# Optimization experiments

Hardware: AMD Instinct MI355X
Metric: run time of the kernel (lower is better)

Reference implementation:

```python
import jax, jax.numpy as jnp
import numpy as np

N_NODES = 100000
N_EDGES = 1600000
IN_CH = 128
DIM = 128
OUT_CH = 10
NUM_GRAPHS = 128
BN_EPS = 1e-5


def _bn_train(h, gamma, beta):
    # BatchNorm1d in training mode: batch statistics over the node axis
    mean = jnp.mean(h, axis=0)
    var = jnp.var(h, axis=0)
    return (h - mean) * jax.lax.rsqrt(var + BN_EPS) * gamma + beta


def _gin_conv(x, src, dst, W1, b1, gamma, beta, W2, b2):
    # GINConv with eps=0: nn(x + sum_{j in N(i)} x_j)
    agg = jax.ops.segment_sum(x[src], dst, num_segments=x.shape[0])  # [N, d]
    h = (x + agg) @ W1 + b1
    h = jax.nn.relu(_bn_train(h, gamma, beta))
    h = jax.nn.relu(h @ W2 + b2)
    return h


def setup_inputs() -> dict:
    key = jax.random.key(0)
    ks = jax.random.split(key, 16)
    s = 0.02
    inp = {
        "x": jax.random.normal(ks[0], (N_NODES, IN_CH), dtype=jnp.float32),
        "edge_index": jax.random.randint(ks[1], (2, N_EDGES), 0, N_NODES, dtype=jnp.int64),
        "batch": jnp.sort(jax.random.randint(ks[2], (N_NODES,), 0, NUM_GRAPHS, dtype=jnp.int64)),
        # conv1 MLP
        "W1a": jax.random.normal(ks[3], (IN_CH, DIM), dtype=jnp.float32) * s,
        "b1a": jnp.zeros((DIM,), jnp.float32),
        "ga": jnp.ones((DIM,), jnp.float32),
        "ba": jnp.zeros((DIM,), jnp.float32),
        "W2a": jax.random.normal(ks[4], (DIM, DIM), dtype=jnp.float32) * s,
        "b2a": jnp.zeros((DIM,), jnp.float32),
        # conv2 MLP
        "W1b": jax.random.normal(ks[5], (DIM, DIM), dtype=jnp.float32) * s,
        "b1b": jnp.zeros((DIM,), jnp.float32),
        "gb": jnp.ones((DIM,), jnp.float32),
        "bb": jnp.zeros((DIM,), jnp.float32),
        "W2b": jax.random.normal(ks[6], (DIM, DIM), dtype=jnp.float32) * s,
        "b2b": jnp.zeros((DIM,), jnp.float32),
        # readout linears
        "Wl1": jax.random.normal(ks[7], (DIM, DIM), dtype=jnp.float32) * s,
        "bl1": jnp.zeros((DIM,), jnp.float32),
        "Wl2": jax.random.normal(ks[8], (DIM, OUT_CH), dtype=jnp.float32) * s,
        "bl2": jnp.zeros((OUT_CH,), jnp.float32),
    }
    return inp


def reference(x, edge_index, batch, W1a, b1a, ga, ba, W2a, b2a,
              W1b, b1b, gb, bb, W2b, b2b, Wl1, bl1, Wl2, bl2):
    src, dst = edge_index[0], edge_index[1]
    h = _gin_conv(x, src, dst, W1a, b1a, ga, ba, W2a, b2a)
    h = _gin_conv(h, src, dst, W1b, b1b, gb, bb, W2b, b2b)
    pooled = jax.ops.segment_sum(h, batch, num_segments=NUM_GRAPHS)  # [G, d]
    out = jax.nn.relu(pooled @ Wl1 + bl1)
    # dropout p=0.5 is identity in deterministic/eval evaluation
    out = out @ Wl2 + bl2
    return out
```

## Files before the change

### kernel.cpp

```cpp
#include <hip/hip_runtime.h>

#define N_NODES    100000
#define N_EDGES    1600000
#define DIM        128
#define OUT_CH     10
#define NUM_GRAPHS 128
#define BN_EPS     1e-5f

#define BSHIFT   10
#define NB       98
#define CAP      24576
#define SLICES   3
#define SLICE_SLOTS 8192

typedef __attribute__((ext_vector_type(8))) short short8;
typedef __attribute__((ext_vector_type(4))) float floatx4;

__device__ inline float bf2f(unsigned short u) {
    union { unsigned i; float f; } v; v.i = (unsigned)u << 16; return v.f;
}
__device__ inline unsigned short f2bf(float f) {
    union { float f; unsigned i; } v; v.f = f;
    unsigned r = (v.i + 0x7fffu + ((v.i >> 16) & 1u)) >> 16;
    return (unsigned short)r;
}

__global__ __launch_bounds__(256)
void k_bucket(const int* __restrict__ src, const int* __restrict__ dst,
              int* __restrict__ gcur, uint2* __restrict__ pairs) {
    __shared__ int h[NB];
    int t = threadIdx.x;
    if (t < NB) h[t] = 0;
    __syncthreads();
    int base = blockIdx.x * 4096;
    #pragma unroll
    for (int i = 0; i < 16; ++i) {
        int idx = base + i * 256 + t;
        if (idx < N_EDGES) atomicAdd(&h[dst[idx] >> BSHIFT], 1);
    }
    __syncthreads();
    if (t < NB) h[t] = atomicAdd(&gcur[t], h[t]);
    __syncthreads();
    #pragma unroll
    for (int i = 0; i < 16; ++i) {
        int idx = base + i * 256 + t;
        if (idx < N_EDGES) {
            int d = dst[idx];
            int b = d >> BSHIFT;
            int pos = atomicAdd(&h[b], 1);
            if (pos < CAP) pairs[(size_t)b * CAP + pos] = make_uint2((unsigned)src[idx], (unsigned)d);
        }
    }
}

__global__ __launch_bounds__(256)
void k_count2(const uint2* __restrict__ pairs, const int* __restrict__ gcur,
              int* __restrict__ cnt) {
    __shared__ int lc[1024];
    int bi = blockIdx.x / SLICES, s = blockIdx.x % SLICES;
    int t = threadIdx.x;
    for (int i = t; i < 1024; i += 256) lc[i] = 0;
    __syncthreads();
    int n  = min(gcur[bi], CAP);
    int lo = s * SLICE_SLOTS, hi = min(lo + SLICE_SLOTS, n);
    const uint2* P = pairs + (size_t)bi * CAP;
    for (int i = lo + t; i < hi; i += 256)
        atomicAdd(&lc[P[i].y & 1023], 1);
    __syncthreads();
    int nb0 = bi << BSHIFT;
    for (int i = t; i < 1024; i += 256)
        if (lc[i] > 0) atomicAdd(&cnt[nb0 + i], lc[i]);
}

__global__ __launch_bounds__(256)
void k_fill2(const uint2* __restrict__ pairs, const int* __restrict__ gcur,
             int* __restrict__ cursor, int* __restrict__ col) {
    __shared__ int lc[1024];
    __shared__ int lb[1024];
    int bi = blockIdx.x / SLICES, s = blockIdx.x % SLICES;
    int t = threadIdx.x;
    for (int i = t; i < 1024; i += 256) lc[i] = 0;
    __syncthreads();
    int n  = min(gcur[bi], CAP);
    int lo = s * SLICE_SLOTS, hi = min(lo + SLICE_SLOTS, n);
    const uint2* P = pairs + (size_t)bi * CAP;
    int nb0 = bi << BSHIFT;
    for (int i = lo + t; i < hi; i += 256)
        atomicAdd(&lc[P[i].y & 1023], 1);
    __syncthreads();
    for (int i = t; i < 1024; i += 256)
        lb[i] = (lc[i] > 0) ? atomicAdd(&cursor[nb0 + i], lc[i]) : 0;
    __syncthreads();
    for (int i = lo + t; i < hi; i += 256) {
        uint2 e = P[i];
        int p = atomicAdd(&lb[e.y & 1023], 1);
        col[p] = (int)e.x;
    }
}

__global__ void k_scanA(const int* __restrict__ cnt, int* __restrict__ outv,
                        int* __restrict__ bsum) {
    __shared__ int sh[256];
    int t = threadIdx.x;
    int base = blockIdx.x * 1024 + t * 4;
    int v0=0,v1=0,v2=0,v3=0;
    if (base+0 < N_NODES) v0 = cnt[base+0];
    if (base+1 < N_NODES) v1 = cnt[base+1];
    if (base+2 < N_NODES) v2 = cnt[base+2];
    if (base+3 < N_NODES) v3 = cnt[base+3];
    int s = v0+v1+v2+v3;
    sh[t] = s; __syncthreads();
    for (int off = 1; off < 256; off <<= 1) {
        int tmp = (t >= off) ? sh[t-off] : 0;
        __syncthreads();
        sh[t] += tmp;
        __syncthreads();
    }
    int excl = sh[t] - s;
    if (t == 255) bsum[blockIdx.x] = sh[255];
    int run = excl;
    if (base+0 < N_NODES) { outv[base+0] = run; run += v0; }
    if (base+1 < N_NODES) { outv[base+1] = run; run += v1; }
    if (base+2 < N_NODES) { outv[base+2] = run; run += v2; }
    if (base+3 < N_NODES) { outv[base+3] = run; run += v3; }
}

__global__ void k_scanB(int* __restrict__ bsum, int* __restrict__ row_ptr) {
    if (threadIdx.x == 0 && blockIdx.x == 0) {
        int run = 0;
        for (int i = 0; i < 98; ++i) { int v = bsum[i]; bsum[i] = run; run += v; }
        row_ptr[N_NODES] = run;
    }
}

__global__ void k_scanC(int* __restrict__ row_ptr, const int* __restrict__ bsum,
                        int* __restrict__ cursor) {
    int i = blockIdx.x * 256 + threadIdx.x;
    if (i < N_NODES) {
        int v = row_ptr[i] + bsum[i >> 10];
        row_ptr[i] = v;
        cursor[i]  = v;
    }
}

__global__ void k_cvt_x(const float* __restrict__ x, unsigned short* __restrict__ xb) {
    int idx = blockIdx.x * 256 + threadIdx.x;
    float4 v = ((const float4*)x)[idx];
    ushort4 o;
    o.x = f2bf(v.x); o.y = f2bf(v.y); o.z = f2bf(v.z); o.w = f2bf(v.w);
    ((ushort4*)xb)[idx] = o;
}

__global__ void k_prep_w(const float* __restrict__ W0, const float* __restrict__ W1,
                         const float* __restrict__ W2, const float* __restrict__ W3,
                         unsigned short* __restrict__ Wt) {
    const float* Ws[4] = {W0, W1, W2, W3};
    const float* W = Ws[blockIdx.y];
    unsigned short* o = Wt + blockIdx.y * (DIM * DIM);
    int idx = blockIdx.x * 256 + threadIdx.x;
    int n = idx >> 7, k = idx & 127;
    o[idx] = f2bf(W[k * DIM + n]);
}

__global__ void k_agg(const unsigned short* __restrict__ X,
                      unsigned short* __restrict__ Out,
                      const int* __restrict__ row_ptr, const int* __restrict__ col) {
    int wid = (blockIdx.x * 256 + threadIdx.x) >> 6;
    if (wid >= N_NODES) return;
    int lane = threadIdx.x & 63;
    int half = lane >> 5, m = lane & 31;
    const ushort4* X4 = (const ushort4*)X;

    float a0=0.f,a1=0.f,a2=0.f,a3=0.f;
    float c0=0.f,c1=0.f,c2=0.f,c3=0.f;
    if (half == 0) {
        ushort4 sv = X4[(size_t)wid * 32 + m];
        a0 = bf2f(sv.x); a1 = bf2f(sv.y); a2 = bf2f(sv.z); a3 = bf2f(sv.w);
    }
    int s = row_ptr[wid], e = row_ptr[wid + 1];
    int p = s + half;
    for (; p + 6 < e; p += 8) {
        int n0 = col[p], n1 = col[p + 2], n2 = col[p + 4], n3 = col[p + 6];
        ushort4 v0 = X4[(size_t)n0 * 32 + m];
        ushort4 v1 = X4[(size_t)n1 * 32 + m];
        ushort4 v2 = X4[(size_t)n2 * 32 + m];
        ushort4 v3 = X4[(size_t)n3 * 32 + m];
        a0 += bf2f(v0.x); a1 += bf2f(v0.y); a2 += bf2f(v0.z); a3 += bf2f(v0.w);
        c0 += bf2f(v1.x); c1 += bf2f(v1.y); c2 += bf2f(v1.z); c3 += bf2f(v1.w);
        a0 += bf2f(v2.x); a1 += bf2f(v2.y); a2 += bf2f(v2.z); a3 += bf2f(v2.w);
        c0 += bf2f(v3.x); c1 += bf2f(v3.y); c2 += bf2f(v3.z); c3 += bf2f(v3.w);
    }
    for (; p < e; p += 2) {
        ushort4 v = X4[(size_t)col[p] * 32 + m];
        a0 += bf2f(v.x); a1 += bf2f(v.y); a2 += bf2f(v.z); a3 += bf2f(v.w);
    }
    a0 += c0; a1 += c1; a2 += c2; a3 += c3;
    a0 += __shfl_xor(a0, 32);
    a1 += __shfl_xor(a1, 32);
    a2 += __shfl_xor(a2, 32);
    a3 += __shfl_xor(a3, 32);
    if (half == 0) {
        ushort4 o;
        o.x = f2bf(a0); o.y = f2bf(a1); o.z = f2bf(a2); o.w = f2bf(a3);
        ((ushort4*)Out)[(size_t)wid * 32 + m] = o;
    }
}

template<bool BN_LOAD, bool RELU_ST>
__global__ __launch_bounds__(256)
void k_gemm(const unsigned short* __restrict__ In, unsigned short* __restrict__ Out,
            const unsigned short* __restrict__ Wt, const float* __restrict__ bias,
            const float* __restrict__ scale, const float* __restrict__ shift) {
    __shared__ __align__(16) unsigned short sA[128][136];
    __shared__ __align__(16) unsigned short sB[128][136];

    int t  = threadIdx.x;
    int r0 = blockIdx.x * 128;

    #pragma unroll
    for (int u = 0; u < 8; ++u) {
        int f   = u * 256 + t;
        int row = f >> 4, kq = f & 15;
        int gr  = r0 + row;
        short8 v = {};
        if (gr < N_NODES) v = *(const short8*)(In + (size_t)gr * 128 + kq * 8);
        if (BN_LOAD) {
            #pragma unroll
            for (int j = 0; j < 8; ++j) {
                int k = kq * 8 + j;
                float fv = bf2f((unsigned short)v[j]);
                fv = fmaxf(fv * scale[k] + shift[k], 0.f);
                v[j] = (short)f2bf(fv);
            }
        }
        *(short8*)&sA[row][kq * 8] = v;
    }
    #pragma unroll
    for (int u = 0; u < 8; ++u) {
        int f = u * 256 + t;
        int n = f >> 4, kq = f & 15;
        *(short8*)&sB[n][kq * 8] = *(const short8*)(Wt + n * 128 + kq * 8);
    }
    __syncthreads();

    int wave = t >> 6;
    int lane = t & 63;
    int m = lane & 15;
    int q = lane >> 4;

    floatx4 acc[2][8] = {};
    #pragma unroll
    for (int kc = 0; kc < 128; kc += 32) {
        short8 n0 = *(const short8*)&sA[wave * 32 + m     ][kc + q * 8];
        short8 n1 = *(const short8*)&sA[wave * 32 + 16 + m][kc + q * 8];
        #pragma unroll
        for (int c = 0; c < 8; ++c) {
            short8 wf = *(const short8*)&sB[c * 16 + m][kc + q * 8];
            acc[0][c] = __builtin_amdgcn_mfma_f32_16x16x32_bf16(wf, n0, acc[0][c], 0, 0, 0);
            acc[1][c] = __builtin_amdgcn_mfma_f32_16x16x32_bf16(wf, n1, acc[1][c], 0, 0, 0);
        }
    }

    #pragma unroll
    for (int c = 0; c < 8; ++c) {
        int ch0 = c * 16 + q * 4;
        float4 bv = *(const float4*)(bias + ch0);
        #pragma unroll
        for (int h = 0; h < 2; ++h) {
            int node = r0 + wave * 32 + h * 16 + m;
            if (node < N_NODES) {
                float v0 = acc[h][c][0] + bv.x;
                float v1 = acc[h][c][1] + bv.y;
                float v2 = acc[h][c][2] + bv.z;
                float v3 = acc[h][c][3] + bv.w;
                if (RELU_ST) {
                    v0 = fmaxf(v0, 0.f); v1 = fmaxf(v1, 0.f);
                    v2 = fmaxf(v2, 0.f); v3 = fmaxf(v3, 0.f);
                }
                ushort4 o;
                o.x = f2bf(v0); o.y = f2bf(v1); o.z = f2bf(v2); o.w = f2bf(v3);
                *(ushort4*)(Out + (size_t)node * 128 + ch0) = o;
            }
        }
    }
}

#define ST_BLOCKS 250
#define ST_ROWS   400
__global__ __launch_bounds__(256)
void k_stats(const unsigned short* __restrict__ H,
             float* __restrict__ ssum, float* __restrict__ ssq) {
    __shared__ float rs[8][128];
    __shared__ float rq[8][128];
    int t  = threadIdx.x;
    int cq = t & 31;
    int r  = t >> 5;
    int row0 = blockIdx.x * ST_ROWS;
    float s0=0,s1=0,s2=0,s3=0,q0=0,q1=0,q2=0,q3=0;
    for (int i = r; i < ST_ROWS; i += 8) {
        ushort4 v = *(const ushort4*)(H + (size_t)(row0 + i) * 128 + cq * 4);
        float f0=bf2f(v.x), f1=bf2f(v.y), f2=bf2f(v.z), f3=bf2f(v.w);
        s0+=f0; s1+=f1; s2+=f2; s3+=f3;
        q0+=f0*f0; q1+=f1*f1; q2+=f2*f2; q3+=f3*f3;
    }
    rs[r][cq*4+0]=s0; rs[r][cq*4+1]=s1; rs[r][cq*4+2]=s2; rs[r][cq*4+3]=s3;
    rq[r][cq*4+0]=q0; rq[r][cq*4+1]=q1; rq[r][cq*4+2]=q2; rq[r][cq*4+3]=q3;
    __syncthreads();
    if (t < 128) {
        float a = 0.f, b = 0.f;
        #pragma unroll
        for (int j = 0; j < 8; ++j) { a += rs[j][t]; b += rq[j][t]; }
        atomicAdd(&ssum[t], a);
        atomicAdd(&ssq [t], b);
    }
}

__global__ void k_bnfin(const float* __restrict__ sum, const float* __restrict__ sq,
                        const float* __restrict__ gamma, const float* __restrict__ beta,
                        float* __restrict__ scale, float* __restrict__ shift) {
    int c = threadIdx.x;
    if (c < DIM) {
        float m   = sum[c] * (1.0f / N_NODES);
        float var = sq[c] * (1.0f / N_NODES) - m * m;
        float inv = rsqrtf(var + BN_EPS);
        float sc  = gamma[c] * inv;
        scale[c] = sc;
        shift[c] = beta[c] - m * sc;
    }
}

#define POOL_BLOCKS 512
#define POOL_CHUNK  196
__global__ void k_pool(const unsigned short* __restrict__ h, const int* __restrict__ batch,
                       float* __restrict__ pooled) {
    int c  = threadIdx.x;
    int n0 = blockIdx.x * POOL_CHUNK;
    if (n0 >= N_NODES) return;
    int n1 = min(n0 + POOL_CHUNK, N_NODES);
    int g = batch[n0];
    float acc = 0.f;
    for (int i = n0; i < n1; ++i) {
        int gi = batch[i];
        if (gi != g) { atomicAdd(&pooled[g * DIM + c], acc); acc = 0.f; g = gi; }
        acc += bf2f(h[(size_t)i * DIM + c]);
    }
    atomicAdd(&pooled[g * DIM + c], acc);
}

__global__ void k_readout1(const float* __restrict__ pooled, const float* __restrict__ W,
                           const float* __restrict__ b, float* __restrict__ r1) {
    int idx = blockIdx.x * 256 + threadIdx.x;
    int g = idx >> 7, c = idx & 127;
    float s = b[c];
    const float* p = pooled + g * DIM;
    #pragma unroll 8
    for (int k = 0; k < DIM; ++k) s += p[k] * W[k * DIM + c];
    r1[idx] = fmaxf(s, 0.f);
}

__global__ void k_readout2(const float* __restrict__ r1, const float* __restrict__ W,
                           const float* __restrict__ b, float* __restrict__ out) {
    int idx = blockIdx.x * 256 + threadIdx.x;
    if (idx >= NUM_GRAPHS * OUT_CH) return;
    int g = idx / OUT_CH, c = idx % OUT_CH;
    float s = b[c];
    const float* r = r1 + g * DIM;
    #pragma unroll 8
    for (int k = 0; k < DIM; ++k) s += r[k] * W[k * OUT_CH + c];
    out[idx] = s;
}

extern "C" void kernel_launch(void* const* d_in, const int* in_sizes, int n_in,
                              void* d_out, int out_size, void* d_ws, size_t ws_size,
                              hipStream_t stream) {
    const float* x   = (const float*)d_in[0];
    const int*   ei  = (const int*)d_in[1];
    const int*   bat = (const int*)d_in[2];
    const float* W1a = (const float*)d_in[3];
    const float* b1a = (const float*)d_in[4];
    const float* ga  = (const float*)d_in[5];
    const float* ba  = (const float*)d_in[6];
    const float* W2a = (const float*)d_in[7];
    const float* b2a = (const float*)d_in[8];
    const float* W1b = (const float*)d_in[9];
    const float* b1b = (const float*)d_in[10];
    const float* gb  = (const float*)d_in[11];
    const float* bbt = (const float*)d_in[12];
    const float* W2b = (const float*)d_in[13];
    const float* b2b = (const float*)d_in[14];
    const float* Wl1 = (const float*)d_in[15];
    const float* bl1 = (const float*)d_in[16];
    const float* Wl2 = (const float*)d_in[17];
    const float* bl2 = (const float*)d_in[18];
    float* out = (float*)d_out;

    const int* src = ei;
    const int* dst = ei + N_EDGES;

    char* w = (char*)d_ws;
    size_t off = 0;
    auto alloc = [&](size_t bytes) -> char* {
        char* p = w + off; off += (bytes + 255) & ~(size_t)255; return p;
    };
    unsigned short* xb   = (unsigned short*)alloc((size_t)N_NODES * DIM * 2);
    unsigned short* nb0  = (unsigned short*)alloc((size_t)N_NODES * DIM * 2);
    unsigned short* nb1  = (unsigned short*)alloc((size_t)N_NODES * DIM * 2);
    unsigned short* Wtb  = (unsigned short*)alloc((size_t)4 * DIM * DIM * 2);
    uint2* pairs   = (uint2*)alloc((size_t)NB * CAP * 8);
    int*   row_ptr = (int*)  alloc((size_t)(N_NODES + 1) * 4);
    int*   cnt     = (int*)  alloc((size_t)(NB * 1024) * 4);
    int*   cursor  = (int*)  alloc((size_t)N_NODES * 4);
    int*   col     = (int*)  alloc((size_t)N_EDGES * 4);
    int*   gcur    = (int*)  alloc(NB * 4);
    int*   bsum    = (int*)  alloc(98 * 4);
    float* ssumA   = (float*)alloc(DIM * 4);
    float* ssqA    = (float*)alloc(DIM * 4);
    float* ssumB   = (float*)alloc(DIM * 4);
    float* ssqB    = (float*)alloc(DIM * 4);
    float* scale   = (float*)alloc(DIM * 4);
    float* shift   = (float*)alloc(DIM * 4);
    float* pooled  = (float*)alloc((size_t)NUM_GRAPHS * DIM * 4);
    float* r1      = (float*)alloc((size_t)NUM_GRAPHS * DIM * 4);

    hipMemsetAsync(gcur,  0, NB * 4, stream);
    hipMemsetAsync(cnt,   0, (size_t)(NB * 1024) * 4, stream);
    hipMemsetAsync(ssumA, 0, DIM * 4 * 4, stream);
    hipMemsetAsync(pooled,0, (size_t)NUM_GRAPHS * DIM * 4, stream);

    k_bucket<<<(N_EDGES + 4095) / 4096, 256, 0, stream>>>(src, dst, gcur, pairs);
    k_count2<<<NB * SLICES, 256, 0, stream>>>(pairs, gcur, cnt);
    k_scanA<<<98, 256, 0, stream>>>(cnt, row_ptr, bsum);
    k_scanB<<<1, 64, 0, stream>>>(bsum, row_ptr);
    k_scanC<<<(N_NODES + 255) / 256, 256, 0, stream>>>(row_ptr, bsum, cursor);
    k_fill2<<<NB * SLICES, 256, 0, stream>>>(pairs, gcur, cursor, col);

    k_cvt_x<<<(N_NODES * DIM / 4) / 256, 256, 0, stream>>>(x, xb);
    k_prep_w<<<dim3(64, 4), 256, 0, stream>>>(W1a, W2a, W1b, W2b, Wtb);
    const unsigned short* Wt1a = Wtb;
    const unsigned short* Wt2a = Wtb + DIM * DIM;
    const unsigned short* Wt1b = Wtb + 2 * DIM * DIM;
    const unsigned short* Wt2b = Wtb + 3 * DIM * DIM;

    int agg_blocks  = (N_NODES * 64) / 256;
    int gemm_blocks = (N_NODES + 127) / 128;

    k_agg<<<agg_blocks, 256, 0, stream>>>(xb, nb0, row_ptr, col);
    k_gemm<false, false><<<gemm_blocks, 256, 0, stream>>>(nb0, nb1, Wt1a, b1a,
                                                          nullptr, nullptr);
    k_stats<<<ST_BLOCKS, 256, 0, stream>>>(nb1, ssumA, ssqA);
    k_bnfin<<<1, 128, 0, stream>>>(ssumA, ssqA, ga, ba, scale, shift);
    k_gemm<true, true><<<gemm_blocks, 256, 0, stream>>>(nb1, nb0, Wt2a, b2a,
                                                        scale, shift);
    k_agg<<<agg_blocks, 256, 0, stream>>>(nb0, nb1, row_ptr, col);
    k_gemm<false, false><<<gemm_blocks, 256, 0, stream>>>(nb1, nb0, Wt1b, b1b,
                                                          nullptr, nullptr);
    k_stats<<<ST_BLOCKS, 256, 0, stream>>>(nb0, ssumB, ssqB);
    k_bnfin<<<1, 128, 0, stream>>>(ssumB, ssqB, gb, bbt, scale, shift);
    k_gemm<true, true><<<gemm_blocks, 256, 0, stream>>>(nb0, nb1, Wt2b, b2b,
                                                        scale, shift);
    k_pool<<<POOL_BLOCKS, 128, 0, stream>>>(nb1, bat, pooled);
    k_readout1<<<(NUM_GRAPHS * DIM) / 256, 256, 0, stream>>>(pooled, Wl1, bl1, r1);
    k_readout2<<<(NUM_GRAPHS * OUT_CH + 255) / 256, 256, 0, stream>>>(r1, Wl2, bl2, out);
}
```

Measured before the change: 536.3 us.

## Simplify CSR build with finer buckets and async swizzled LDS loads in GEMM

New measurement: 526.3 us. No clear change (-1.9%).

```diff
diff --git a/kernel.cpp b/kernel.cpp
--- a/kernel.cpp
+++ b/kernel.cpp
@@ -7,11 +7,9 @@
 #define NUM_GRAPHS 128
 #define BN_EPS     1e-5f
 
-#define BSHIFT   10
-#define NB       98
-#define CAP      24576
-#define SLICES   3
-#define SLICE_SLOTS 8192
+#define BSHIFT   8
+#define NB2      391
+#define CAP2     5120
 
 typedef __attribute__((ext_vector_type(8))) short short8;
 typedef __attribute__((ext_vector_type(4))) float floatx4;
@@ -25,12 +23,18 @@
     return (unsigned short)r;
 }
 
+__device__ inline void async_cp16(const unsigned short* g, unsigned short* l) {
+    __builtin_amdgcn_global_load_lds(
+        (const __attribute__((address_space(1))) void*)g,
+        (__attribute__((address_space(3))) void*)l, 16, 0, 0);
+}
+
 __global__ __launch_bounds__(256)
 void k_bucket(const int* __restrict__ src, const int* __restrict__ dst,
               int* __restrict__ gcur, uint2* __restrict__ pairs) {
-    __shared__ int h[NB];
+    __shared__ int h[NB2];
     int t = threadIdx.x;
-    if (t < NB) h[t] = 0;
+    for (int i = t; i < NB2; i += 256) h[i] = 0;
     __syncthreads();
     int base = blockIdx.x * 4096;
     #pragma unroll
@@ -39,7 +43,7 @@
         if (idx < N_EDGES) atomicAdd(&h[dst[idx] >> BSHIFT], 1);
     }
     __syncthreads();
-    if (t < NB) h[t] = atomicAdd(&gcur[t], h[t]);
+    for (int i = t; i < NB2; i += 256) h[i] = atomicAdd(&gcur[i], h[i]);
     __syncthreads();
     #pragma unroll
     for (int i = 0; i < 16; ++i) {
@@ -48,98 +52,59 @@
             int d = dst[idx];
             int b = d >> BSHIFT;
             int pos = atomicAdd(&h[b], 1);
-            if (pos < CAP) pairs[(size_t)b * CAP + pos] = make_uint2((unsigned)src[idx], (unsigned)d);
+            if (pos < CAP2) pairs[(size_t)b * CAP2 + pos] = make_uint2((unsigned)src[idx], (unsigned)d);
         }
     }
 }
 
-__global__ __launch_bounds__(256)
-void k_count2(const uint2* __restrict__ pairs, const int* __restrict__ gcur,
-              int* __restrict__ cnt) {
-    __shared__ int lc[1024];
-    int bi = blockIdx.x / SLICES, s = blockIdx.x % SLICES;
+__global__ void k_bscan(const int* __restrict__ gcur, int* __restrict__ bbase,
+                        int* __restrict__ row_ptr) {
+    __shared__ int sh[512];
     int t = threadIdx.x;
-    for (int i = t; i < 1024; i += 256) lc[i] = 0;
-    __syncthreads();
-    int n  = min(gcur[bi], CAP);
-    int lo = s * SLICE_SLOTS, hi = min(lo + SLICE_SLOTS, n);
-    const uint2* P = pairs + (size_t)bi * CAP;
-    for (int i = lo + t; i < hi; i += 256)
-        atomicAdd(&lc[P[i].y & 1023], 1);
-    __syncthreads();
-    int nb0 = bi << BSHIFT;
-    for (int i = t; i < 1024; i += 256)
-        if (lc[i] > 0) atomicAdd(&cnt[nb0 + i], lc[i]);
-}
-
-__global__ __launch_bounds__(256)
-void k_fill2(const uint2* __restrict__ pairs, const int* __restrict__ gcur,
-             int* __restrict__ cursor, int* __restrict__ col) {
-    __shared__ int lc[1024];
-    __shared__ int lb[1024];
-    int bi = blockIdx.x / SLICES, s = blockIdx.x % SLICES;
-    int t = threadIdx.x;
-    for (int i = t; i < 1024; i += 256) lc[i] = 0;
-    __syncthreads();
-    int n  = min(gcur[bi], CAP);
-    int lo = s * SLICE_SLOTS, hi = min(lo + SLICE_SLOTS, n);
-    const uint2* P = pairs + (size_t)bi * CAP;
-    int nb0 = bi << BSHIFT;
-    for (int i = lo + t; i < hi; i += 256)
-        atomicAdd(&lc[P[i].y & 1023], 1);
-    __syncthreads();
-    for (int i = t; i < 1024; i += 256)
-        lb[i] = (lc[i] > 0) ? atomicAdd(&cursor[nb0 + i], lc[i]) : 0;
-    __syncthreads();
-    for (int i = lo + t; i < hi; i += 256) {
-        uint2 e = P[i];
-        int p = atomicAdd(&lb[e.y & 1023], 1);
-        col[p] = (int)e.x;
-    }
-}
-
-__global__ void k_scanA(const int* __restrict__ cnt, int* __restrict__ outv,
-                        int* __restrict__ bsum) {
-    __shared__ int sh[256];
-    int t = threadIdx.x;
-    int base = blockIdx.x * 1024 + t * 4;
-    int v0=0,v1=0,v2=0,v3=0;
-    if (base+0 < N_NODES) v0 = cnt[base+0];
-    if (base+1 < N_NODES) v1 = cnt[base+1];
-    if (base+2 < N_NODES) v2 = cnt[base+2];
-    if (base+3 < N_NODES) v3 = cnt[base+3];
-    int s = v0+v1+v2+v3;
-    sh[t] = s; __syncthreads();
-    for (int off = 1; off < 256; off <<= 1) {
-        int tmp = (t >= off) ? sh[t-off] : 0;
+    int v = (t < NB2) ? min(gcur[t], CAP2) : 0;
+    sh[t] = v; __syncthreads();
+    for (int off = 1; off < 512; off <<= 1) {
+        int tmp = (t >= off) ? sh[t - off] : 0;
         __syncthreads();
         sh[t] += tmp;
         __syncthreads();
     }
-    int excl = sh[t] - s;
-    if (t == 255) bsum[blockIdx.x] = sh[255];
-    int run = excl;
-    if (base+0 < N_NODES) { outv[base+0] = run; run += v0; }
-    if (base+1 < N_NODES) { outv[base+1] = run; run += v1; }
-    if (base+2 < N_NODES) { outv[base+2] = run; run += v2; }
-    if (base+3 < N_NODES) { outv[base+3] = run; run += v3; }
-}
-
-__global__ void k_scanB(int* __restrict__ bsum, int* __restrict__ row_ptr) {
-    if (threadIdx.x == 0 && blockIdx.x == 0) {
-        int run = 0;
-        for (int i = 0; i < 98; ++i) { int v = bsum[i]; bsum[i] = run; run += v; }
-        row_ptr[N_NODES] = run;
-    }
-}
-
-__global__ void k_scanC(int* __restrict__ row_ptr, const int* __restrict__ bsum,
-                        int* __restrict__ cursor) {
-    int i = blockIdx.x * 256 + threadIdx.x;
-    if (i < N_NODES) {
-        int v = row_ptr[i] + bsum[i >> 10];
-        row_ptr[i] = v;
-        cursor[i]  = v;
+    if (t < NB2) bbase[t] = sh[t] - v;
+    if (t == NB2 - 1) { bbase[NB2] = sh[t]; row_ptr[N_NODES] = sh[t]; }
+}
+
+__global__ __launch_bounds__(256)
+void k_csr(const uint2* __restrict__ pairs, const int* __restrict__ gcur,
+           const int* __restrict__ bbase, int* __restrict__ row_ptr,
+           int* __restrict__ col) {
+    __shared__ int hist[256];
+    __shared__ int cur[256];
+    int bi = blockIdx.x, t = threadIdx.x;
+    hist[t] = 0; __syncthreads();
+    int n = min(gcur[bi], CAP2);
+    const uint2* P = pairs + (size_t)bi * CAP2;
+    for (int i = t; i < n; i += 256)
+        atomicAdd(&hist[P[i].y & 255], 1);
+    __syncthreads();
+    int self = hist[t];
+    cur[t] = self; __syncthreads();
+    for (int off = 1; off < 256; off <<= 1) {
+        int tmp = (t >= off) ? cur[t - off] : 0;
+        __syncthreads();
+        cur[t] += tmp;
+        __syncthreads();
+    }
+    int excl = cur[t] - self;
+    int base = bbase[bi];
+    int node = (bi << 8) + t;
+    if (node < N_NODES) row_ptr[node] = base + excl;
+    __syncthreads();
+    cur[t] = base + excl;
+    __syncthreads();
+    for (int i = t; i < n; i += 256) {
+        uint2 e = P[i];
+        int pos = atomicAdd(&cur[e.y & 255], 1);
+        col[pos] = (int)e.x;
     }
 }
 
@@ -206,58 +171,52 @@
     }
 }
 
-template<bool BN_LOAD, bool RELU_ST>
+template<bool RELU_ST>
 __global__ __launch_bounds__(256)
 void k_gemm(const unsigned short* __restrict__ In, unsigned short* __restrict__ Out,
-            const unsigned short* __restrict__ Wt, const float* __restrict__ bias,
-            const float* __restrict__ scale, const float* __restrict__ shift) {
-    __shared__ __align__(16) unsigned short sA[128][136];
-    __shared__ __align__(16) unsigned short sB[128][136];
-
-    int t  = threadIdx.x;
+            const unsigned short* __restrict__ Wt, const float* __restrict__ bias) {
+    __shared__ __align__(16) unsigned short sA[128 * 128];
+    __shared__ __align__(16) unsigned short sB[128 * 128];
+
+    int t = threadIdx.x;
+    int w = t >> 6, lane = t & 63;
     int r0 = blockIdx.x * 128;
 
     #pragma unroll
     for (int u = 0; u < 8; ++u) {
-        int f   = u * 256 + t;
-        int row = f >> 4, kq = f & 15;
-        int gr  = r0 + row;
-        short8 v = {};
-        if (gr < N_NODES) v = *(const short8*)(In + (size_t)gr * 128 + kq * 8);
-        if (BN_LOAD) {
-            #pragma unroll
-            for (int j = 0; j < 8; ++j) {
-                int k = kq * 8 + j;
-                float fv = bf2f((unsigned short)v[j]);
-                fv = fmaxf(fv * scale[k] + shift[k], 0.f);
-                v[j] = (short)f2bf(fv);
-            }
-        }
-        *(short8*)&sA[row][kq * 8] = v;
+        int i = (w * 8 + u) * 64 + lane;
+        int row = i >> 4, p = i & 15;
+        int gr = r0 + row; if (gr >= N_NODES) gr = 0;
+        const unsigned short* g = In + (size_t)gr * 128 + ((p ^ (row & 7)) << 3);
+        async_cp16(g, sA + (size_t)(w * 8 + u) * 512);
     }
     #pragma unroll
     for (int u = 0; u < 8; ++u) {
-        int f = u * 256 + t;
-        int n = f >> 4, kq = f & 15;
-        *(short8*)&sB[n][kq * 8] = *(const short8*)(Wt + n * 128 + kq * 8);
-    }
-    __syncthreads();
-
-    int wave = t >> 6;
-    int lane = t & 63;
+        int i = (w * 8 + u) * 64 + lane;
+        int n = i >> 4, p = i & 15;
+        const unsigned short* g = Wt + n * 128 + ((p ^ (n & 7)) << 3);
+        async_cp16(g, sB + (size_t)(w * 8 + u) * 512);
+    }
+    __syncthreads();
+
     int m = lane & 15;
     int q = lane >> 4;
+    int sw = m & 7;
 
     floatx4 acc[2][8] = {};
-    #pragma unroll
-    for (int kc = 0; kc < 128; kc += 32) {
-        short8 n0 = *(const short8*)&sA[wave * 32 + m     ][kc + q * 8];
-        short8 n1 = *(const short8*)&sA[wave * 32 + 16 + m][kc + q * 8];
+    int rA0 = w * 32 + m, rA1 = w * 32 + 16 + m;
+    #pragma unroll
+    for (int kk = 0; kk < 4; ++kk) {
+        int cl = kk * 4 + q;
+        int cp = cl ^ sw;
+        short8 a0 = *(const short8*)&sA[rA0 * 128 + (cp << 3)];
+        short8 a1 = *(const short8*)&sA[rA1 * 128 + (cp << 3)];
         #pragma unroll
         for (int c = 0; c < 8; ++c) {
-            short8 wf = *(const short8*)&sB[c * 16 + m][kc + q * 8];
-            acc[0][c] = __builtin_amdgcn_mfma_f32_16x16x32_bf16(wf, n0, acc[0][c], 0, 0, 0);
-            acc[1][c] = __builtin_amdgcn_mfma_f32_16x16x32_bf16(wf, n1, acc[1][c], 0, 0, 0);
+            int nr = c * 16 + m;
+            short8 b = *(const short8*)&sB[nr * 128 + (cp << 3)];
+            acc[0][c] = __builtin_amdgcn_mfma_f32_16x16x32_bf16(b, a0, acc[0][c], 0, 0, 0);
+            acc[1][c] = __builtin_amdgcn_mfma_f32_16x16x32_bf16(b, a1, acc[1][c], 0, 0, 0);
         }
     }
 
@@ -267,7 +226,7 @@
         float4 bv = *(const float4*)(bias + ch0);
         #pragma unroll
         for (int h = 0; h < 2; ++h) {
-            int node = r0 + wave * 32 + h * 16 + m;
+            int node = r0 + w * 32 + h * 16 + m;
             if (node < N_NODES) {
                 float v0 = acc[h][c][0] + bv.x;
                 float v1 = acc[h][c][1] + bv.y;
@@ -327,6 +286,25 @@
         scale[c] = sc;
         shift[c] = beta[c] - m * sc;
     }
+}
+
+__global__ __launch_bounds__(256)
+void k_bn_apply(unsigned short* __restrict__ H, const float* __restrict__ scale,
+                const float* __restrict__ shift) {
+    __shared__ float ssc[128], ssh[128];
+    int t = threadIdx.x;
+    if (t < 128) { ssc[t] = scale[t]; ssh[t] = shift[t]; }
+    __syncthreads();
+    size_t idx = (size_t)blockIdx.x * 256 + t;
+    int k0 = ((int)idx & 15) * 8;
+    short8 v = ((short8*)H)[idx];
+    #pragma unroll
+    for (int j = 0; j < 8; ++j) {
+        float f = bf2f((unsigned short)v[j]);
+        f = fmaxf(f * ssc[k0 + j] + ssh[k0 + j], 0.f);
+        v[j] = (short)f2bf(f);
+    }
+    ((short8*)H)[idx] = v;
 }
 
 #define POOL_BLOCKS 512
@@ -406,13 +384,11 @@
     unsigned short* nb0  = (unsigned short*)alloc((size_t)N_NODES * DIM * 2);
     unsigned short* nb1  = (unsigned short*)alloc((size_t)N_NODES * DIM * 2);
     unsigned short* Wtb  = (unsigned short*)alloc((size_t)4 * DIM * DIM * 2);
-    uint2* pairs   = (uint2*)alloc((size_t)NB * CAP * 8);
+    uint2* pairs   = (uint2*)alloc((size_t)NB2 * CAP2 * 8);
     int*   row_ptr = (int*)  alloc((size_t)(N_NODES + 1) * 4);
-    int*   cnt     = (int*)  alloc((size_t)(NB * 1024) * 4);
-    int*   cursor  = (int*)  alloc((size_t)N_NODES * 4);
     int*   col     = (int*)  alloc((size_t)N_EDGES * 4);
-    int*   gcur    = (int*)  alloc(NB * 4);
-    int*   bsum    = (int*)  alloc(98 * 4);
+    int*   gcur    = (int*)  alloc((NB2 + 1) * 4);
+    int*   bbase   = (int*)  alloc((NB2 + 1) * 4);
     float* ssumA   = (float*)alloc(DIM * 4);
     float* ssqA    = (float*)alloc(DIM * 4);
     float* ssumB   = (float*)alloc(DIM * 4);
@@ -422,17 +398,13 @@
     float* pooled  = (float*)alloc((size_t)NUM_GRAPHS * DIM * 4);
     float* r1      = (float*)alloc((size_t)NUM_GRAPHS * DIM * 4);
 
-    hipMemsetAsync(gcur,  0, NB * 4, stream);
-    hipMemsetAsync(cnt,   0, (size_t)(NB * 1024) * 4, stream);
+    hipMemsetAsync(gcur,  0, (NB2 + 1) * 4, stream);
     hipMemsetAsync(ssumA, 0, DIM * 4 * 4, stream);
     hipMemsetAsync(pooled,0, (size_t)NUM_GRAPHS * DIM * 4, stream);
 
     k_bucket<<<(N_EDGES + 4095) / 4096, 256, 0, stream>>>(src, dst, gcur, pairs);
-    k_count2<<<NB * SLICES, 256, 0, stream>>>(pairs, gcur, cnt);
-    k_scanA<<<98, 256, 0, stream>>>(cnt, row_ptr, bsum);
-    k_scanB<<<1, 64, 0, stream>>>(bsum, row_ptr);
-    k_scanC<<<(N_NODES + 255) / 256, 256, 0, stream>>>(row_ptr, bsum, cursor);
-    k_fill2<<<NB * SLICES, 256, 0, stream>>>(pairs, gcur, cursor, col);
+    k_bscan<<<1, 512, 0, stream>>>(gcur, bbase, row_ptr);
+    k_csr<<<NB2, 256, 0, stream>>>(pairs, gcur, bbase, row_ptr, col);
 
     k_cvt_x<<<(N_NODES * DIM / 4) / 256, 256, 0, stream>>>(x, xb);
     k_prep_w<<<dim3(64, 4), 256, 0, stream>>>(W1a, W2a, W1b, W2b, Wtb);
@@ -443,21 +415,20 @@
 
     int agg_blocks  = (N_NODES * 64) / 256;
     int gemm_blocks = (N_NODES + 127) / 128;
+    int bn_blocks   = (N_NODES * DIM / 8) / 256;
 
     k_agg<<<agg_blocks, 256, 0, stream>>>(xb, nb0, row_ptr, col);
-    k_gemm<false, false><<<gemm_blocks, 256, 0, stream>>>(nb0, nb1, Wt1a, b1a,
-                                                          nullptr, nullptr);
+    k_gemm<false><<<gemm_blocks, 256, 0, stream>>>(nb0, nb1, Wt1a, b1a);
     k_stats<<<ST_BLOCKS, 256, 0, stream>>>(nb1, ssumA, ssqA);
     k_bnfin<<<1, 128, 0, stream>>>(ssumA, ssqA, ga, ba, scale, shift);
-    k_gemm<true, true><<<gemm_blocks, 256, 0, stream>>>(nb1, nb0, Wt2a, b2a,
-                                                        scale, shift);
+    k_bn_apply<<<bn_blocks, 256, 0, stream>>>(nb1, scale, shift);
+    k_gemm<true><<<gemm_blocks, 256, 0, stream>>>(nb1, nb0, Wt2a, b2a);
     k_agg<<<agg_blocks, 256, 0, stream>>>(nb0, nb1, row_ptr, col);
-    k_gemm<false, false><<<gemm_blocks, 256, 0, stream>>>(nb1, nb0, Wt1b, b1b,
-                                                          nullptr, nullptr);
+    k_gemm<false><<<gemm_blocks, 256, 0, stream>>>(nb1, nb0, Wt1b, b1b);
     k_stats<<<ST_BLOCKS, 256, 0, stream>>>(nb0, ssumB, ssqB);
     k_bnfin<<<1, 128, 0, stream>>>(ssumB, ssqB, gb, bbt, scale, shift);
-    k_gemm<true, true><<<gemm_blocks, 256, 0, stream>>>(nb0, nb1, Wt2b, b2b,
-                                                        scale, shift);
+    k_bn_apply<<<bn_blocks, 256, 0, stream>>>(nb0, scale, shift);
+    k_gemm<true><<<gemm_blocks, 256, 0, stream>>>(nb0, nb1, Wt2b, b2b);
     k_pool<<<POOL_BLOCKS, 128, 0, stream>>>(nb1, bat, pooled);
     k_readout1<<<(NUM_GRAPHS * DIM) / 256, 256, 0, stream>>>(pooled, Wl1, bl1, r1);
     k_readout2<<<(NUM_GRAPHS * OUT_CH + 255) / 256, 256, 0, stream>>>(r1, Wl2, bl2, out);
```
